# Performance work log

Hardware: AMD Instinct MI355X
Metric: run time of the kernel (lower is better)

## Reference

```python
import jax, jax.numpy as jnp
import numpy as np

N_GRAPHS = 64
HEADS = 8
HEAD_DIM = 16  # hidden_dim // heads
HIDDEN = 128
N_LAYERS = 4


def _layer_norm(x, g, b, eps=1e-5):
    mu = jnp.mean(x, axis=-1, keepdims=True)
    var = jnp.var(x, axis=-1, keepdims=True)
    return (x - mu) * jax.lax.rsqrt(var + eps) * g + b


def _transformer_conv(h, src, tgt, Wq, bq, Wk, bk, Wv, bv, Ws, bs, Wbeta):
    # PyG TransformerConv, heads concat, beta=True, root_weight=True, eval (no dropout)
    N = h.shape[0]
    q = (h @ Wq.T + bq).reshape(N, HEADS, HEAD_DIM)
    k = (h @ Wk.T + bk).reshape(N, HEADS, HEAD_DIM)
    v = (h @ Wv.T + bv).reshape(N, HEADS, HEAD_DIM)
    # attention scores per edge: messages flow src -> tgt (query at tgt)
    scores = jnp.sum(q[tgt] * k[src], axis=-1) / jnp.sqrt(jnp.float32(HEAD_DIM))  # [E, H]
    # segment softmax over incoming edges of each target node
    m = jnp.full((N, HEADS), -jnp.inf, dtype=scores.dtype).at[tgt].max(scores)
    m = jnp.where(jnp.isfinite(m), m, 0.0)
    p = jnp.exp(scores - m[tgt])  # [E, H]
    denom = jax.ops.segment_sum(p, tgt, num_segments=N)  # [N, H]
    alpha = p / jnp.maximum(denom[tgt], 1e-16)
    agg = jax.ops.segment_sum(alpha[..., None] * v[src], tgt, num_segments=N)  # [N, H, d]
    out = agg.reshape(N, HIDDEN)
    # root/skip + beta gating
    r = h @ Ws.T + bs  # [N, HIDDEN]
    beta = jax.nn.sigmoid(jnp.concatenate([out, r, out - r], axis=-1) @ Wbeta.T)  # [N, 1]
    return beta * r + (1.0 - beta) * out


def _forward(x, edge_index, batch, Win, b_in, Wq, bq, Wk, bk, Wv, bv, Ws, bs, Wbeta, ln_g, ln_b):
    src, tgt = edge_index[0], edge_index[1]
    h = x @ Win.T + b_in
    for l in range(N_LAYERS):
        h_new = _transformer_conv(h, src, tgt, Wq[l], bq[l], Wk[l], bk[l], Wv[l], bv[l], Ws[l], bs[l], Wbeta[l])
        h = _layer_norm(h + h_new, ln_g[l], ln_b[l])
        # dropout: eval mode -> identity
    N = h.shape[0]
    ones = jnp.ones((N,), dtype=h.dtype)
    counts = jax.ops.segment_sum(ones, batch, num_segments=N_GRAPHS)
    sums = jax.ops.segment_sum(h, batch, num_segments=N_GRAPHS)
    local_repr = sums / jnp.maximum(counts, 1.0)[:, None]
    gmax = jnp.full((N_GRAPHS, HIDDEN), -jnp.inf, dtype=h.dtype).at[batch].max(h)
    global_repr = jnp.where(jnp.isfinite(gmax), gmax, 0.0)
    return local_repr, global_repr, h


def setup_inputs() -> dict:
    key = jax.random.key(0)
    ks = jax.random.split(key, 20)
    N, E, F_IN = 50000, 800000, 64
    s = 0.05
    inp = {
        'x': jax.random.normal(ks[0], (N, F_IN), dtype=jnp.float32),
        'edge_index': jax.random.randint(ks[1], (2, E), 0, N, dtype=jnp.int64),
        'batch': jnp.sort(jax.random.randint(ks[2], (N,), 0, N_GRAPHS, dtype=jnp.int64)),
        'Win': jax.random.normal(ks[3], (HIDDEN, F_IN), dtype=jnp.float32) * s,
        'b_in': jnp.zeros((HIDDEN,), dtype=jnp.float32),
        'Wq': jax.random.normal(ks[4], (N_LAYERS, HIDDEN, HIDDEN), dtype=jnp.float32) * s,
        'bq': jnp.zeros((N_LAYERS, HIDDEN), dtype=jnp.float32),
        'Wk': jax.random.normal(ks[5], (N_LAYERS, HIDDEN, HIDDEN), dtype=jnp.float32) * s,
        'bk': jnp.zeros((N_LAYERS, HIDDEN), dtype=jnp.float32),
        'Wv': jax.random.normal(ks[6], (N_LAYERS, HIDDEN, HIDDEN), dtype=jnp.float32) * s,
        'bv': jnp.zeros((N_LAYERS, HIDDEN), dtype=jnp.float32),
        'Ws': jax.random.normal(ks[7], (N_LAYERS, HIDDEN, HIDDEN), dtype=jnp.float32) * s,
        'bs': jnp.zeros((N_LAYERS, HIDDEN), dtype=jnp.float32),
        'Wbeta': jax.random.normal(ks[8], (N_LAYERS, 1, 3 * HIDDEN), dtype=jnp.float32) * s,
        'ln_g': jnp.ones((N_LAYERS, HIDDEN), dtype=jnp.float32),
        'ln_b': jnp.zeros((N_LAYERS, HIDDEN), dtype=jnp.float32),
    }
    return inp


def reference(x, edge_index, batch, Win, b_in, Wq, bq, Wk, bk, Wv, bv, Ws, bs, Wbeta, ln_g, ln_b):
    return _forward(x, edge_index, batch, Win, b_in, Wq, bq, Wk, bk, Wv, bv, Ws, bs, Wbeta, ln_g, ln_b)
```

## Files before the change

kernel.cpp:

```cpp
#include <hip/hip_runtime.h>
#include <math.h>

#define HID 128
#define NG 64
#define NLAYERS 4
#define PCHUNK 128

typedef __attribute__((ext_vector_type(8))) short bf16x8;
typedef __attribute__((ext_vector_type(4))) float f32x4;


static __device__ __forceinline__ float wave_sum64(float x) {
#pragma unroll
  for (int w = 1; w < 64; w <<= 1) x += __shfl_xor(x, w);
  return x;
}

static __device__ __forceinline__ int wave_sum64_i(int x) {
#pragma unroll
  for (int w = 1; w < 64; w <<= 1) x += __shfl_xor(x, w);
  return x;
}

static __device__ __forceinline__ unsigned enc_f(float f) {
  unsigned u = __float_as_uint(f);
  return (u & 0x80000000u) ? ~u : (u | 0x80000000u);
}
#define ENC_NEG_INF 0x007FFFFFu
static __device__ __forceinline__ float dec_f(unsigned e) {
  unsigned u = (e & 0x80000000u) ? (e & 0x7FFFFFFFu) : ~e;
  return __uint_as_float(u);
}

static __device__ __forceinline__ unsigned short f2bf(float x) {
  unsigned u = __float_as_uint(x);
  unsigned r = (u + 0x7FFFu + ((u >> 16) & 1u)) >> 16;
  return (unsigned short)r;
}
static __device__ __forceinline__ float bf2f(unsigned short b) {
  return __uint_as_float((unsigned)b << 16);
}


__global__ void hist_kernel(const int* __restrict__ tgt, int* __restrict__ cnt, int E) {
  int i = blockIdx.x * blockDim.x + threadIdx.x;
  if (i < E) atomicAdd(&cnt[tgt[i]], 1);
}

__global__ __launch_bounds__(1024) void block_sum_kernel(const int* __restrict__ cnt,
                                                         int* __restrict__ bsum, int N) {
  __shared__ int red[16];
  int i = blockIdx.x * 1024 + threadIdx.x;
  int x = (i < N) ? cnt[i] : 0;
  x = wave_sum64_i(x);
  if ((threadIdx.x & 63) == 0) red[threadIdx.x >> 6] = x;
  __syncthreads();
  if (threadIdx.x < 16) {
    int y = red[threadIdx.x];
#pragma unroll
    for (int w = 1; w < 16; w <<= 1) y += __shfl_xor(y, w);
    if (threadIdx.x == 0) bsum[blockIdx.x] = y;
  }
}

__global__ __launch_bounds__(1024) void scan_bsum_kernel(int* __restrict__ bsum, int NB) {
  __shared__ int lds[1024];
  int t = threadIdx.x;
  int x = (t < NB) ? bsum[t] : 0;
  lds[t] = x;
  __syncthreads();
#pragma unroll
  for (int ofs = 1; ofs < 1024; ofs <<= 1) {
    int y = (t >= ofs) ? lds[t - ofs] : 0;
    __syncthreads();
    lds[t] += y;
    __syncthreads();
  }
  if (t < NB) bsum[t] = lds[t] - x;
}

__global__ __launch_bounds__(1024) void scan_final_kernel(const int* __restrict__ cnt,
                                                          const int* __restrict__ bsum,
                                                          int* __restrict__ off, int N) {
  __shared__ int lds[1024];
  int t = threadIdx.x;
  int i = blockIdx.x * 1024 + t;
  int x = (i < N) ? cnt[i] : 0;
  lds[t] = x;
  __syncthreads();
#pragma unroll
  for (int ofs = 1; ofs < 1024; ofs <<= 1) {
    int y = (t >= ofs) ? lds[t - ofs] : 0;
    __syncthreads();
    lds[t] += y;
    __syncthreads();
  }
  if (i < N) off[i + 1] = lds[t] + bsum[blockIdx.x];
  if (i == 0) off[0] = 0;
}

__global__ void scatter_kernel(const int* __restrict__ src, const int* __restrict__ tgt,
                               const int* __restrict__ off, int* __restrict__ fill,
                               int* __restrict__ ssrc, int E) {
  int i = blockIdx.x * blockDim.x + threadIdx.x;
  if (i < E) {
    int tg = tgt[i];
    int pos = off[tg] + atomicAdd(&fill[tg], 1);
    ssrc[pos] = src[i];
  }
}


__global__ void prep_w(const float* __restrict__ Wq, const float* __restrict__ Wk,
                       const float* __restrict__ Wv, const float* __restrict__ Ws,
                       unsigned short* __restrict__ w_hi, unsigned short* __restrict__ w_lo) {
  int b = blockIdx.x;
  int l = b >> 2, t = b & 3;
  const float* W = (t == 0 ? Wq : t == 1 ? Wk : t == 2 ? Wv : Ws) + (size_t)l * HID * HID;
  size_t base = (size_t)b * HID * HID;
  for (int i = threadIdx.x; i < HID * HID; i += blockDim.x) {
    float x = W[i];
    unsigned short hi = f2bf(x);
    w_hi[base + i] = hi;
    w_lo[base + i] = f2bf(x - bf2f(hi));
  }
}

__global__ void transpose_in(const float* __restrict__ Win, float* __restrict__ wtin, int FIN) {
  for (int i = threadIdx.x + blockIdx.x * blockDim.x; i < HID * FIN;
       i += blockDim.x * gridDim.x) {
    int oo = i / FIN, kk = i % FIN;
    wtin[(size_t)kk * HID + oo] = Win[i];
  }
}

__global__ void split_h(const float* __restrict__ h, unsigned short* __restrict__ hh,
                        unsigned short* __restrict__ hl, int total) {
  int i = blockIdx.x * blockDim.x + threadIdx.x;
  if (i < total) {
    float x = h[i];
    unsigned short hi = f2bf(x);
    hh[i] = hi;
    hl[i] = f2bf(x - bf2f(hi));
  }
}


template <int K>
static __device__ __forceinline__ void gemm_core(const float* __restrict__ A,
                                                 const float* __restrict__ Wt,
                                                 const float* __restrict__ bias,
                                                 float* __restrict__ C, int N,
                                                 float (*As)[132], float (*Bs)[HID]) {
  const int tid = threadIdx.x;
  const int tx = tid & 15, ty = tid >> 4;
  const int row0 = blockIdx.x * 128;
  float acc[2][4][2][4] = {};

  for (int k0 = 0; k0 < K; k0 += 64) {
#pragma unroll
    for (int i = 0; i < 8; ++i) {
      int lin = i * 256 + tid;
      int row = lin >> 4;
      int kq = lin & 15;
      float4 val = make_float4(0.f, 0.f, 0.f, 0.f);
      int grow = row0 + row;
      if (grow < N) val = *(const float4*)(A + (size_t)grow * K + k0 + kq * 4);
      As[kq * 4 + 0][row] = val.x;
      As[kq * 4 + 1][row] = val.y;
      As[kq * 4 + 2][row] = val.z;
      As[kq * 4 + 3][row] = val.w;
    }
#pragma unroll
    for (int i = 0; i < 8; ++i) {
      int lin = i * 256 + tid;
      int kk = lin >> 5;
      int oq = lin & 31;
      *(float4*)&Bs[kk][oq * 4] = *(const float4*)(Wt + (size_t)(k0 + kk) * HID + oq * 4);
    }
    __syncthreads();
#pragma unroll 4
    for (int kk = 0; kk < 64; ++kk) {
      float4 a0 = *(const float4*)&As[kk][ty * 4];
      float4 a1 = *(const float4*)&As[kk][64 + ty * 4];
      float4 b0 = *(const float4*)&Bs[kk][tx * 4];
      float4 b1 = *(const float4*)&Bs[kk][64 + tx * 4];
      float a[2][4] = {{a0.x, a0.y, a0.z, a0.w}, {a1.x, a1.y, a1.z, a1.w}};
      float b[2][4] = {{b0.x, b0.y, b0.z, b0.w}, {b1.x, b1.y, b1.z, b1.w}};
#pragma unroll
      for (int rb = 0; rb < 2; ++rb)
#pragma unroll
        for (int rr = 0; rr < 4; ++rr)
#pragma unroll
          for (int cb = 0; cb < 2; ++cb)
#pragma unroll
            for (int cc = 0; cc < 4; ++cc)
              acc[rb][rr][cb][cc] += a[rb][rr] * b[cb][cc];
    }
    __syncthreads();
  }
#pragma unroll
  for (int rb = 0; rb < 2; ++rb)
#pragma unroll
    for (int rr = 0; rr < 4; ++rr) {
      int grow = row0 + rb * 64 + ty * 4 + rr;
      if (grow >= N) continue;
#pragma unroll
      for (int cb = 0; cb < 2; ++cb) {
        int col = cb * 64 + tx * 4;
        float4 o;
        o.x = acc[rb][rr][cb][0] + bias[col + 0];
        o.y = acc[rb][rr][cb][1] + bias[col + 1];
        o.z = acc[rb][rr][cb][2] + bias[col + 2];
        o.w = acc[rb][rr][cb][3] + bias[col + 3];
        *(float4*)(C + (size_t)grow * HID + col) = o;
      }
    }
}

__global__ __launch_bounds__(256) void gemm_in_kernel(const float* __restrict__ A,
                                                      const float* __restrict__ Wt,
                                                      const float* __restrict__ bias,
                                                      float* __restrict__ C, int N) {
  __shared__ float As[64][132];
  __shared__ float Bs[64][HID];
  gemm_core<64>(A, Wt, bias, C, N, As, Bs);
}

__global__ __launch_bounds__(256) void gemm4_mfma(
    const unsigned short* __restrict__ h_hi, const unsigned short* __restrict__ h_lo,
    const unsigned short* __restrict__ w_hi4, const unsigned short* __restrict__ w_lo4,
    const float* __restrict__ bq, const float* __restrict__ bk,
    const float* __restrict__ bv, const float* __restrict__ bs,
    float* __restrict__ qkvr, int N) {
  const int yt = blockIdx.y;
  const unsigned short* Whi = w_hi4 + (size_t)yt * HID * HID;
  const unsigned short* Wlo = w_lo4 + (size_t)yt * HID * HID;
  const float* bias = (yt == 0) ? bq : (yt == 1) ? bk : (yt == 2) ? bv : bs;
  float* C = qkvr + (size_t)yt * N * HID;

  __shared__ __align__(16) unsigned short AsH[64][HID];
  __shared__ __align__(16) unsigned short AsL[64][HID];

  const int tid = threadIdx.x;
  const int rowblk = blockIdx.x * 64;

#pragma unroll
  for (int i = 0; i < 8; ++i) {
    int lin = i * 256 + tid;
    int buf = lin >> 10;
    int r = (lin >> 4) & 63;
    int g = lin & 15;
    int grow = rowblk + r;
    if (grow >= N) grow = N - 1;
    const unsigned short* src = (buf ? h_lo : h_hi) + (size_t)grow * HID + g * 8;
    bf16x8 val = *(const bf16x8*)src;
    int gs = g ^ (r & 7);
    if (buf)
      *(bf16x8*)&AsL[r][gs * 8] = val;
    else
      *(bf16x8*)&AsH[r][gs * 8] = val;
  }
  __syncthreads();

  const int w = tid >> 6;
  const int l = tid & 63;
  const int l15 = l & 15, lg = l >> 4;

  const int rw = (w & 1) * 32;
  const int colbase = (w >> 1) * 64;

  f32x4 acc[2][4] = {};

#pragma unroll
  for (int ks = 0; ks < 4; ++ks) {
    const int kb = ks * 32 + lg * 8;
    const int gr = ks * 4 + lg;
    bf16x8 ahi[2], alo[2];
#pragma unroll
    for (int mt = 0; mt < 2; ++mt) {
      int rl = rw + mt * 16 + l15;
      int gs = gr ^ (rl & 7);
      ahi[mt] = *(const bf16x8*)&AsH[rl][gs * 8];
      alo[mt] = *(const bf16x8*)&AsL[rl][gs * 8];
    }
#pragma unroll
    for (int nt = 0; nt < 4; ++nt) {
      const int col = colbase + nt * 16 + l15;
      bf16x8 bhi = *(const bf16x8*)(Whi + (size_t)col * HID + kb);
      bf16x8 blo = *(const bf16x8*)(Wlo + (size_t)col * HID + kb);
#pragma unroll
      for (int mt = 0; mt < 2; ++mt) {
        acc[mt][nt] = __builtin_amdgcn_mfma_f32_16x16x32_bf16(ahi[mt], bhi, acc[mt][nt], 0, 0, 0);
        acc[mt][nt] = __builtin_amdgcn_mfma_f32_16x16x32_bf16(ahi[mt], blo, acc[mt][nt], 0, 0, 0);
        acc[mt][nt] = __builtin_amdgcn_mfma_f32_16x16x32_bf16(alo[mt], bhi, acc[mt][nt], 0, 0, 0);
      }
    }
  }

#pragma unroll
  for (int mt = 0; mt < 2; ++mt) {
#pragma unroll
    for (int reg = 0; reg < 4; ++reg) {
      int grow = rowblk + rw + mt * 16 + lg * 4 + reg;
      if (grow >= N) continue;
#pragma unroll
      for (int nt = 0; nt < 4; ++nt) {
        int gcol = colbase + nt * 16 + l15;
        C[(size_t)grow * HID + gcol] = acc[mt][nt][reg] + bias[gcol];
      }
    }
  }
}


__global__ __launch_bounds__(128) void attn_layer(const float* __restrict__ qkvr,
                                                  const int* __restrict__ off,
                                                  const int* __restrict__ ssrc,
                                                  const float* __restrict__ Wb,
                                                  const float* __restrict__ g,
                                                  const float* __restrict__ b,
                                                  float* __restrict__ h,
                                                  unsigned short* __restrict__ hh,
                                                  unsigned short* __restrict__ hl, int N) {
  int n = blockIdx.x;
  int d = threadIdx.x;
  const float* q = qkvr;
  const float* k = qkvr + (size_t)N * HID;
  const float* v = qkvr + 2 * (size_t)N * HID;
  const float* r = qkvr + 3 * (size_t)N * HID;

  float qd = q[(size_t)n * HID + d];
  int e0 = off[n], e1 = off[n + 1];

  float s = 0.f, acc = 0.f;
  int e = e0;
  for (; e + 7 < e1; e += 8) {
    int j0 = ssrc[e + 0], j1 = ssrc[e + 1], j2 = ssrc[e + 2], j3 = ssrc[e + 3];
    int j4 = ssrc[e + 4], j5 = ssrc[e + 5], j6 = ssrc[e + 6], j7 = ssrc[e + 7];
    float k0 = k[(size_t)j0 * HID + d], k1 = k[(size_t)j1 * HID + d];
    float k2 = k[(size_t)j2 * HID + d], k3 = k[(size_t)j3 * HID + d];
    float k4 = k[(size_t)j4 * HID + d], k5 = k[(size_t)j5 * HID + d];
    float k6 = k[(size_t)j6 * HID + d], k7 = k[(size_t)j7 * HID + d];
    float v0 = v[(size_t)j0 * HID + d], v1 = v[(size_t)j1 * HID + d];
    float v2 = v[(size_t)j2 * HID + d], v3 = v[(size_t)j3 * HID + d];
    float v4 = v[(size_t)j4 * HID + d], v5 = v[(size_t)j5 * HID + d];
    float v6 = v[(size_t)j6 * HID + d], v7 = v[(size_t)j7 * HID + d];
    float p0 = qd * k0, p1 = qd * k1, p2 = qd * k2, p3 = qd * k3;
    float p4 = qd * k4, p5 = qd * k5, p6 = qd * k6, p7 = qd * k7;
#pragma unroll
    for (int w = 1; w < 16; w <<= 1) {
      p0 += __shfl_xor(p0, w);
      p1 += __shfl_xor(p1, w);
      p2 += __shfl_xor(p2, w);
      p3 += __shfl_xor(p3, w);
      p4 += __shfl_xor(p4, w);
      p5 += __shfl_xor(p5, w);
      p6 += __shfl_xor(p6, w);
      p7 += __shfl_xor(p7, w);
    }
    float w0 = __expf(p0 * 0.25f), w1 = __expf(p1 * 0.25f);
    float w2 = __expf(p2 * 0.25f), w3 = __expf(p3 * 0.25f);
    float w4 = __expf(p4 * 0.25f), w5 = __expf(p5 * 0.25f);
    float w6 = __expf(p6 * 0.25f), w7 = __expf(p7 * 0.25f);
    s += ((w0 + w1) + (w2 + w3)) + ((w4 + w5) + (w6 + w7));
    acc += w0 * v0;
    acc += w1 * v1;
    acc += w2 * v2;
    acc += w3 * v3;
    acc += w4 * v4;
    acc += w5 * v5;
    acc += w6 * v6;
    acc += w7 * v7;
  }
  for (; e < e1; ++e) {
    int j = ssrc[e];
    float kd = k[(size_t)j * HID + d];
    float vd = v[(size_t)j * HID + d];
    float p = qd * kd;
#pragma unroll
    for (int w = 1; w < 16; w <<= 1) p += __shfl_xor(p, w);
    float w_ = __expf(p * 0.25f);
    s += w_;
    acc += w_ * vd;
  }

  float out = acc / fmaxf(s, 1e-16f);
  float rd = r[(size_t)n * HID + d];

  float c = Wb[d] * out + Wb[HID + d] * rd + Wb[2 * HID + d] * (out - rd);
  __shared__ float red1[2];
  float cs = wave_sum64(c);
  if ((d & 63) == 0) red1[d >> 6] = cs;
  __syncthreads();
  float logit = red1[0] + red1[1];
  float beta = 1.f / (1.f + __expf(-logit));
  float hn = beta * rd + (1.f - beta) * out;
  float t = h[(size_t)n * HID + d] + hn;

  __shared__ float red2[2][2];
  float ssum = wave_sum64(t);
  float ssq = wave_sum64(t * t);
  if ((d & 63) == 0) { red2[d >> 6][0] = ssum; red2[d >> 6][1] = ssq; }
  __syncthreads();
  float mu = (red2[0][0] + red2[1][0]) * (1.f / HID);
  float ms = (red2[0][1] + red2[1][1]) * (1.f / HID);
  float var = ms - mu * mu;
  float y = (t - mu) * rsqrtf(var + 1e-5f) * g[d] + b[d];
  h[(size_t)n * HID + d] = y;
  unsigned short hi = f2bf(y);
  hh[(size_t)n * HID + d] = hi;
  hl[(size_t)n * HID + d] = f2bf(y - bf2f(hi));
}


__global__ void pool_init(float* __restrict__ sums, unsigned* __restrict__ enc,
                          int* __restrict__ counts) {
  int i = blockIdx.x * blockDim.x + threadIdx.x;
  if (i < NG * HID) {
    sums[i] = 0.f;
    enc[i] = ENC_NEG_INF;
  }
  if (i < NG) counts[i] = 0;
}

__global__ __launch_bounds__(128) void pool_seg(const float* __restrict__ h,
                                                const int* __restrict__ batch,
                                                float* __restrict__ sums,
                                                unsigned* __restrict__ enc,
                                                int* __restrict__ counts, int N) {
  int d = threadIdx.x;
  int n0 = blockIdx.x * PCHUNK;
  int n1 = n0 + PCHUNK;
  if (n1 > N) n1 = N;
  if (n0 >= N) return;
  int cur = batch[n0];
  float s = 0.f, mx = -INFINITY;
  int cn = 0;
  for (int n = n0; n < n1; ++n) {
    int gI = batch[n];
    if (gI != cur) {
      atomicAdd(&sums[cur * HID + d], s);
      atomicMax(&enc[cur * HID + d], enc_f(mx));
      if (d == 0) atomicAdd(&counts[cur], cn);
      s = 0.f;
      mx = -INFINITY;
      cn = 0;
      cur = gI;
    }
    float x = h[(size_t)n * HID + d];
    s += x;
    mx = fmaxf(mx, x);
    ++cn;
  }
  atomicAdd(&sums[cur * HID + d], s);
  atomicMax(&enc[cur * HID + d], enc_f(mx));
  if (d == 0) atomicAdd(&counts[cur], cn);
}

__global__ void pool_fin(const float* __restrict__ sums, const unsigned* __restrict__ enc,
                         const int* __restrict__ counts, float* __restrict__ out) {
  int i = blockIdx.x * blockDim.x + threadIdx.x;
  if (i >= NG * HID) return;
  int gI = i >> 7;
  float cnt = (float)counts[gI];
  out[i] = sums[i] / fmaxf(cnt, 1.f);
  unsigned e = enc[i];
  float gm = (e == ENC_NEG_INF) ? 0.f : dec_f(e);
  out[NG * HID + i] = gm;
}


extern "C" void kernel_launch(void* const* d_in, const int* in_sizes, int n_in, void* d_out,
                              int out_size, void* d_ws, size_t ws_size, hipStream_t stream) {
  const float* x = (const float*)d_in[0];
  const int* ei = (const int*)d_in[1];
  const int* batch = (const int*)d_in[2];
  const float* Win = (const float*)d_in[3];
  const float* b_in = (const float*)d_in[4];
  const float* Wq = (const float*)d_in[5];
  const float* bq = (const float*)d_in[6];
  const float* Wk = (const float*)d_in[7];
  const float* bk = (const float*)d_in[8];
  const float* Wv = (const float*)d_in[9];
  const float* bv = (const float*)d_in[10];
  const float* Ws_ = (const float*)d_in[11];
  const float* bs = (const float*)d_in[12];
  const float* Wbeta = (const float*)d_in[13];
  const float* ln_g = (const float*)d_in[14];
  const float* ln_b = (const float*)d_in[15];

  const int N = in_sizes[2];
  const int E = in_sizes[1] / 2;
  const int FIN = in_sizes[0] / N;

  float* out = (float*)d_out;
  float* h = out + NG * HID * 2;

  char* w = (char*)d_ws;
  auto alloc = [&](size_t bytes) {
    char* p = w;
    w += (bytes + 255) & ~(size_t)255;
    return p;
  };
  float* qkvr = (float*)alloc((size_t)4 * N * HID * 4);
  unsigned short* w_hi = (unsigned short*)alloc((size_t)16 * HID * HID * 2);
  unsigned short* w_lo = (unsigned short*)alloc((size_t)16 * HID * HID * 2);
  unsigned short* h_hi = (unsigned short*)alloc((size_t)N * HID * 2);
  unsigned short* h_lo = (unsigned short*)alloc((size_t)N * HID * 2);
  float* wtin = (float*)alloc((size_t)FIN * HID * 4);
  int* cnt = (int*)alloc((size_t)N * 4);
  int* fill = (int*)alloc((size_t)N * 4);
  int* off = (int*)alloc((size_t)(N + 1) * 4);
  int* ssrc = (int*)alloc((size_t)E * 4);
  int* bsum = (int*)alloc((size_t)1024 * 4);
  float* sums = (float*)alloc(NG * HID * 4);
  unsigned* enc = (unsigned*)alloc(NG * HID * 4);
  int* counts = (int*)alloc(NG * 4);

  hipMemsetAsync(cnt, 0, (size_t)N * 4, stream);
  hipMemsetAsync(fill, 0, (size_t)N * 4, stream);

  const int* esrc = ei;
  const int* etgt = ei + E;

  const int NB = (N + 1023) / 1024;

  hist_kernel<<<(E + 255) / 256, 256, 0, stream>>>(etgt, cnt, E);
  block_sum_kernel<<<NB, 1024, 0, stream>>>(cnt, bsum, N);
  scan_bsum_kernel<<<1, 1024, 0, stream>>>(bsum, NB);
  scan_final_kernel<<<NB, 1024, 0, stream>>>(cnt, bsum, off, N);
  scatter_kernel<<<(E + 255) / 256, 256, 0, stream>>>(esrc, etgt, off, fill, ssrc, E);

  prep_w<<<16, 256, 0, stream>>>(Wq, Wk, Wv, Ws_, w_hi, w_lo);
  transpose_in<<<4, 256, 0, stream>>>(Win, wtin, FIN);

  gemm_in_kernel<<<(N + 127) / 128, 256, 0, stream>>>(x, wtin, b_in, h, N);
  split_h<<<(N * HID + 255) / 256, 256, 0, stream>>>(h, h_hi, h_lo, N * HID);

  for (int l = 0; l < NLAYERS; ++l) {
    gemm4_mfma<<<dim3((N + 63) / 64, 4), 256, 0, stream>>>(
        h_hi, h_lo, w_hi + (size_t)l * 4 * HID * HID, w_lo + (size_t)l * 4 * HID * HID,
        bq + l * HID, bk + l * HID, bv + l * HID, bs + l * HID, qkvr, N);
    attn_layer<<<N, 128, 0, stream>>>(qkvr, off, ssrc, Wbeta + l * 3 * HID, ln_g + l * HID,
                                      ln_b + l * HID, h, h_hi, h_lo, N);
  }

  pool_init<<<(NG * HID + 255) / 256, 256, 0, stream>>>(sums, enc, counts);
  pool_seg<<<(N + PCHUNK - 1) / PCHUNK, 128, 0, stream>>>(h, batch, sums, enc, counts, N);
  pool_fin<<<(NG * HID + 255) / 256, 256, 0, stream>>>(sums, enc, counts, out);
}
```

Baseline: 1.061 ms.

## Store K and V in bf16 for gathers and fuse h split into input GEMM

The QKV GEMM now writes K and V as bf16 instead of fp32, which halves the bytes moved by the per-edge gathers in the attention kernel. Q and the root projection stay in fp32. Separately, the bf16 hi/lo split of the input-projection output now happens in the GEMM epilogue, removing the split_h kernel launch and one extra pass over h. The trade-off is lower precision in the attention scores and values, which may matter for accuracy tolerance.

```diff
diff --git a/kernel.cpp b/kernel.cpp
--- a/kernel.cpp
+++ b/kernel.cpp
@@ -134,23 +134,14 @@
   }
 }
 
-__global__ void split_h(const float* __restrict__ h, unsigned short* __restrict__ hh,
-                        unsigned short* __restrict__ hl, int total) {
-  int i = blockIdx.x * blockDim.x + threadIdx.x;
-  if (i < total) {
-    float x = h[i];
-    unsigned short hi = f2bf(x);
-    hh[i] = hi;
-    hl[i] = f2bf(x - bf2f(hi));
-  }
-}
-
 
 template <int K>
 static __device__ __forceinline__ void gemm_core(const float* __restrict__ A,
                                                  const float* __restrict__ Wt,
                                                  const float* __restrict__ bias,
-                                                 float* __restrict__ C, int N,
+                                                 float* __restrict__ C,
+                                                 unsigned short* __restrict__ hh,
+                                                 unsigned short* __restrict__ hl, int N,
                                                  float (*As)[132], float (*Bs)[HID]) {
   const int tid = threadIdx.x;
   const int tx = tid & 15, ty = tid >> 4;
@@ -214,6 +205,13 @@
         o.z = acc[rb][rr][cb][2] + bias[col + 2];
         o.w = acc[rb][rr][cb][3] + bias[col + 3];
         *(float4*)(C + (size_t)grow * HID + col) = o;
+        float vv[4] = {o.x, o.y, o.z, o.w};
+#pragma unroll
+        for (int q_ = 0; q_ < 4; ++q_) {
+          unsigned short hi = f2bf(vv[q_]);
+          hh[(size_t)grow * HID + col + q_] = hi;
+          hl[(size_t)grow * HID + col + q_] = f2bf(vv[q_] - bf2f(hi));
+        }
       }
     }
 }
@@ -221,10 +219,12 @@
 __global__ __launch_bounds__(256) void gemm_in_kernel(const float* __restrict__ A,
                                                       const float* __restrict__ Wt,
                                                       const float* __restrict__ bias,
-                                                      float* __restrict__ C, int N) {
+                                                      float* __restrict__ C,
+                                                      unsigned short* __restrict__ hh,
+                                                      unsigned short* __restrict__ hl, int N) {
   __shared__ float As[64][132];
   __shared__ float Bs[64][HID];
-  gemm_core<64>(A, Wt, bias, C, N, As, Bs);
+  gemm_core<64>(A, Wt, bias, C, hh, hl, N, As, Bs);
 }
 
 __global__ __launch_bounds__(256) void gemm4_mfma(
@@ -232,12 +232,12 @@
     const unsigned short* __restrict__ w_hi4, const unsigned short* __restrict__ w_lo4,
     const float* __restrict__ bq, const float* __restrict__ bk,
     const float* __restrict__ bv, const float* __restrict__ bs,
-    float* __restrict__ qkvr, int N) {
+    float* __restrict__ qr, unsigned short* __restrict__ k16,
+    unsigned short* __restrict__ v16, int N) {
   const int yt = blockIdx.y;
   const unsigned short* Whi = w_hi4 + (size_t)yt * HID * HID;
   const unsigned short* Wlo = w_lo4 + (size_t)yt * HID * HID;
   const float* bias = (yt == 0) ? bq : (yt == 1) ? bk : (yt == 2) ? bv : bs;
-  float* C = qkvr + (size_t)yt * N * HID;
 
   __shared__ __align__(16) unsigned short AsH[64][HID];
   __shared__ __align__(16) unsigned short AsL[64][HID];
@@ -298,6 +298,10 @@
     }
   }
 
+  const bool isKV = (yt == 1) || (yt == 2);
+  unsigned short* Ckv = (yt == 1) ? k16 : v16;
+  float* Cf = (yt == 0) ? qr : qr + (size_t)N * HID;
+
 #pragma unroll
   for (int mt = 0; mt < 2; ++mt) {
 #pragma unroll
@@ -307,14 +311,20 @@
 #pragma unroll
       for (int nt = 0; nt < 4; ++nt) {
         int gcol = colbase + nt * 16 + l15;
-        C[(size_t)grow * HID + gcol] = acc[mt][nt][reg] + bias[gcol];
+        float val = acc[mt][nt][reg] + bias[gcol];
+        if (isKV)
+          Ckv[(size_t)grow * HID + gcol] = f2bf(val);
+        else
+          Cf[(size_t)grow * HID + gcol] = val;
       }
     }
   }
 }
 
 
-__global__ __launch_bounds__(128) void attn_layer(const float* __restrict__ qkvr,
+__global__ __launch_bounds__(128) void attn_layer(const float* __restrict__ qr,
+                                                  const unsigned short* __restrict__ k16,
+                                                  const unsigned short* __restrict__ v16,
                                                   const int* __restrict__ off,
                                                   const int* __restrict__ ssrc,
                                                   const float* __restrict__ Wb,
@@ -325,10 +335,8 @@
                                                   unsigned short* __restrict__ hl, int N) {
   int n = blockIdx.x;
   int d = threadIdx.x;
-  const float* q = qkvr;
-  const float* k = qkvr + (size_t)N * HID;
-  const float* v = qkvr + 2 * (size_t)N * HID;
-  const float* r = qkvr + 3 * (size_t)N * HID;
+  const float* q = qr;
+  const float* r = qr + (size_t)N * HID;
 
   float qd = q[(size_t)n * HID + d];
   int e0 = off[n], e1 = off[n + 1];
@@ -338,14 +346,14 @@
   for (; e + 7 < e1; e += 8) {
     int j0 = ssrc[e + 0], j1 = ssrc[e + 1], j2 = ssrc[e + 2], j3 = ssrc[e + 3];
     int j4 = ssrc[e + 4], j5 = ssrc[e + 5], j6 = ssrc[e + 6], j7 = ssrc[e + 7];
-    float k0 = k[(size_t)j0 * HID + d], k1 = k[(size_t)j1 * HID + d];
-    float k2 = k[(size_t)j2 * HID + d], k3 = k[(size_t)j3 * HID + d];
-    float k4 = k[(size_t)j4 * HID + d], k5 = k[(size_t)j5 * HID + d];
-    float k6 = k[(size_t)j6 * HID + d], k7 = k[(size_t)j7 * HID + d];
-    float v0 = v[(size_t)j0 * HID + d], v1 = v[(size_t)j1 * HID + d];
-    float v2 = v[(size_t)j2 * HID + d], v3 = v[(size_t)j3 * HID + d];
-    float v4 = v[(size_t)j4 * HID + d], v5 = v[(size_t)j5 * HID + d];
-    float v6 = v[(size_t)j6 * HID + d], v7 = v[(size_t)j7 * HID + d];
+    float k0 = bf2f(k16[(size_t)j0 * HID + d]), k1 = bf2f(k16[(size_t)j1 * HID + d]);
+    float k2 = bf2f(k16[(size_t)j2 * HID + d]), k3 = bf2f(k16[(size_t)j3 * HID + d]);
+    float k4 = bf2f(k16[(size_t)j4 * HID + d]), k5 = bf2f(k16[(size_t)j5 * HID + d]);
+    float k6 = bf2f(k16[(size_t)j6 * HID + d]), k7 = bf2f(k16[(size_t)j7 * HID + d]);
+    float v0 = bf2f(v16[(size_t)j0 * HID + d]), v1 = bf2f(v16[(size_t)j1 * HID + d]);
+    float v2 = bf2f(v16[(size_t)j2 * HID + d]), v3 = bf2f(v16[(size_t)j3 * HID + d]);
+    float v4 = bf2f(v16[(size_t)j4 * HID + d]), v5 = bf2f(v16[(size_t)j5 * HID + d]);
+    float v6 = bf2f(v16[(size_t)j6 * HID + d]), v7 = bf2f(v16[(size_t)j7 * HID + d]);
     float p0 = qd * k0, p1 = qd * k1, p2 = qd * k2, p3 = qd * k3;
     float p4 = qd * k4, p5 = qd * k5, p6 = qd * k6, p7 = qd * k7;
 #pragma unroll
@@ -375,8 +383,8 @@
   }
   for (; e < e1; ++e) {
     int j = ssrc[e];
-    float kd = k[(size_t)j * HID + d];
-    float vd = v[(size_t)j * HID + d];
+    float kd = bf2f(k16[(size_t)j * HID + d]);
+    float vd = bf2f(v16[(size_t)j * HID + d]);
     float p = qd * kd;
 #pragma unroll
     for (int w = 1; w < 16; w <<= 1) p += __shfl_xor(p, w);
@@ -503,7 +511,9 @@
     w += (bytes + 255) & ~(size_t)255;
     return p;
   };
-  float* qkvr = (float*)alloc((size_t)4 * N * HID * 4);
+  float* qr = (float*)alloc((size_t)2 * N * HID * 4);
+  unsigned short* k16 = (unsigned short*)alloc((size_t)N * HID * 2);
+  unsigned short* v16 = (unsigned short*)alloc((size_t)N * HID * 2);
   unsigned short* w_hi = (unsigned short*)alloc((size_t)16 * HID * HID * 2);
   unsigned short* w_lo = (unsigned short*)alloc((size_t)16 * HID * HID * 2);
   unsigned short* h_hi = (unsigned short*)alloc((size_t)N * HID * 2);
@@ -535,15 +545,14 @@
   prep_w<<<16, 256, 0, stream>>>(Wq, Wk, Wv, Ws_, w_hi, w_lo);
   transpose_in<<<4, 256, 0, stream>>>(Win, wtin, FIN);
 
-  gemm_in_kernel<<<(N + 127) / 128, 256, 0, stream>>>(x, wtin, b_in, h, N);
-  split_h<<<(N * HID + 255) / 256, 256, 0, stream>>>(h, h_hi, h_lo, N * HID);
+  gemm_in_kernel<<<(N + 127) / 128, 256, 0, stream>>>(x, wtin, b_in, h, h_hi, h_lo, N);
 
   for (int l = 0; l < NLAYERS; ++l) {
     gemm4_mfma<<<dim3((N + 63) / 64, 4), 256, 0, stream>>>(
         h_hi, h_lo, w_hi + (size_t)l * 4 * HID * HID, w_lo + (size_t)l * 4 * HID * HID,
-        bq + l * HID, bk + l * HID, bv + l * HID, bs + l * HID, qkvr, N);
-    attn_layer<<<N, 128, 0, stream>>>(qkvr, off, ssrc, Wbeta + l * 3 * HID, ln_g + l * HID,
-                                      ln_b + l * HID, h, h_hi, h_lo, N);
+        bq + l * HID, bk + l * HID, bv + l * HID, bs + l * HID, qr, k16, v16, N);
+    attn_layer<<<N, 128, 0, stream>>>(qr, k16, v16, off, ssrc, Wbeta + l * 3 * HID,
+                                      ln_g + l * HID, ln_b + l * HID, h, h_hi, h_lo, N);
   }
 
   pool_init<<<(NG * HID + 255) / 256, 256, 0, stream>>>(sums, enc, counts);
```

Result: faster. 986.7 us (-7.0%).
